# Optimization experiments

Hardware: AMD Instinct MI355X
Metric: run time of the kernel (lower is better)

## Reference

```python
import jax, jax.numpy as jnp
import numpy as np

ROPE_BASE = 10000.0


def _rope(x):
    # Faithful to the torch module: positions indexed by x.shape[2],
    # which after split_heads is the HEADS axis. x: [B, S, H, D]
    B, S, H, D = x.shape
    theta = 1.0 / (ROPE_BASE ** (jnp.arange(0, D, 2, dtype=x.dtype) / D))  # [D/2]
    pos = jnp.arange(H, dtype=x.dtype)[:, None]  # [H, 1]
    ang = pos * theta  # [H, D/2], broadcasts against [B, S, H, D/2]
    sin, cos = jnp.sin(ang), jnp.cos(ang)
    xe, xo = x[..., 0::2], x[..., 1::2]
    re = xe * cos - xo * sin
    ro = xe * sin + xo * cos
    # interleave back: even slots <- re, odd slots <- ro
    return jnp.stack([re, ro], axis=-1).reshape(B, S, H, D)


def setup_inputs() -> dict:
    key = jax.random.key(0)
    k0, k1, k2, k3 = jax.random.split(key, 4)
    B, S, Dm = 8, 2048, 2048
    scale = 1.0 / np.sqrt(Dm)
    return {
        "x": jax.random.normal(k0, (B, S, Dm), dtype=jnp.float32),
        "Wq": jax.random.normal(k1, (Dm, Dm), dtype=jnp.float32) * scale,
        "Wk": jax.random.normal(k2, (Dm, Dm), dtype=jnp.float32) * scale,
        "Wv": jax.random.normal(k3, (Dm, Dm), dtype=jnp.float32) * scale,
        "st_pos": 0,
    }


def reference(x, Wq, Wk, Wv, st_pos):
    B, S, Dm = x.shape
    H = 16
    D = Dm // H  # head_dim = 128
    q = jnp.einsum("bsd,df->bsf", x, Wq).reshape(B, S, H, D)
    k = jnp.einsum("bsd,df->bsf", x, Wk).reshape(B, S, H, D)
    v = jnp.einsum("bsd,df->bsf", x, Wv).reshape(B, S, H, D)
    q = _rope(q)
    k = _rope(k)
    return q, k, v
```

## Files before the change

kernel.cpp:

```cpp
#include <hip/hip_runtime.h>
#include <hip/hip_bf16.h>
#include <stdint.h>


typedef __attribute__((ext_vector_type(8))) short short8;
typedef __attribute__((ext_vector_type(4))) float f32x4;

__device__ __forceinline__ unsigned short f2bf(float f) {
  __bf16 h = (__bf16)f;
  return __builtin_bit_cast(unsigned short, h);
}

__device__ __forceinline__ void gload_lds16(const void* g, void* l) {
  __builtin_amdgcn_global_load_lds((const __attribute__((address_space(1))) void*)g,
                                   (__attribute__((address_space(3))) void*)l,
                                   16, 0, 0);
}


__global__ __launch_bounds__(256) void convert_x(const float* __restrict__ X,
                                                 unsigned short* __restrict__ Xb,
                                                 int n8) {
  const int stride = gridDim.x * blockDim.x;
  for (int i = blockIdx.x * blockDim.x + threadIdx.x; i < n8; i += stride) {
    const float4 v0 = ((const float4*)X)[(size_t)i * 2 + 0];
    const float4 v1 = ((const float4*)X)[(size_t)i * 2 + 1];
    uint4 w;
    w.x = (uint32_t)f2bf(v0.x) | ((uint32_t)f2bf(v0.y) << 16);
    w.y = (uint32_t)f2bf(v0.z) | ((uint32_t)f2bf(v0.w) << 16);
    w.z = (uint32_t)f2bf(v1.x) | ((uint32_t)f2bf(v1.y) << 16);
    w.w = (uint32_t)f2bf(v1.z) | ((uint32_t)f2bf(v1.w) << 16);
    ((uint4*)Xb)[i] = w;
  }
}

__global__ __launch_bounds__(256) void transpose_cvt(const float* __restrict__ W,
                                                     unsigned short* __restrict__ WT) {
  __shared__ unsigned short tile[64][65];
  const int bx = blockIdx.x * 64;
  const int by = blockIdx.y * 64;
  const int t  = threadIdx.x;
  const int tr = t >> 4;
  const int tc = (t & 15) * 4;
#pragma unroll
  for (int i = 0; i < 4; ++i) {
    const int r = tr + i * 16;
    const float4 v = *(const float4*)&W[(size_t)(by + r) * 2048 + bx + tc];
    tile[r][tc + 0] = f2bf(v.x);
    tile[r][tc + 1] = f2bf(v.y);
    tile[r][tc + 2] = f2bf(v.z);
    tile[r][tc + 3] = f2bf(v.w);
  }
  __syncthreads();
#pragma unroll
  for (int i = 0; i < 4; ++i) {
    const int a = tr + i * 16;
    ushort4 o;
    o.x = tile[tc + 0][a];
    o.y = tile[tc + 1][a];
    o.z = tile[tc + 2][a];
    o.w = tile[tc + 3][a];
    *(ushort4*)&WT[(size_t)(bx + a) * 2048 + by + tc] = o;
  }
}


__global__ __launch_bounds__(512, 2) void qkv_fused9(const unsigned short* __restrict__ Xb,
                                                     const unsigned short* __restrict__ WT,
                                                     float* __restrict__ Out) {
  extern __shared__ char smem[];

  const int wg  = blockIdx.x;
  const int swz = (wg & 7) * 192 + (wg >> 3);
  const int mb  = swz / 24, nb = swz % 24;
  const int m0  = mb * 256, n0 = nb * 256;

  const int tid  = threadIdx.x;
  const int wave = tid >> 6, lane = tid & 63;
  const int l15  = lane & 15, lg = lane >> 4;
  const int wm   = (wave >> 2) * 128;
  const int wn   = (wave & 3) * 64;
  const int s0   = ((lg ^ ((l15 >> 1) & 3)) << 4);

  const unsigned short* Xp = Xb + (size_t)m0 * 2048;
  const unsigned short* Wp = WT + (size_t)n0 * 2048;

  const int srow  = tid >> 2;
  const int sswz  = ((tid & 3) ^ ((tid >> 3) & 3)) << 3;

  f32x4 acc[8][4] = {};

#define STAGE(S)                                                              \
  do {                                                                        \
    const int kt_ = (S) * 32;                                                 \
    char* base_ = smem + ((S) & 3) * 32768;                                   \
    _Pragma("unroll") for (int i = 0; i < 2; ++i) {                           \
      const int row = i * 128 + srow;                                         \
      gload_lds16(Xp + (size_t)row * 2048 + kt_ + sswz,                       \
                  base_ + i * 8192 + tid * 16);                               \
    }                                                                         \
    _Pragma("unroll") for (int i = 0; i < 2; ++i) {                           \
      const int row = i * 128 + srow;                                         \
      gload_lds16(Wp + (size_t)row * 2048 + kt_ + sswz,                       \
                  base_ + 16384 + i * 8192 + tid * 16);                       \
    }                                                                         \
  } while (0)

#define BODY(S, VMCNT_ASM, DO_STAGE)                                          \
  do {                                                                        \
    asm volatile(VMCNT_ASM ::: "memory");                                     \
    __builtin_amdgcn_s_barrier();                                             \
    if (DO_STAGE) STAGE((S) + 3);                                             \
    const char* Ab_ = smem + ((S) & 3) * 32768;                               \
    const char* Bb_ = Ab_ + 16384;                                            \
    short8 bf[4], af[8];                                                      \
    _Pragma("unroll") for (int ni = 0; ni < 4; ++ni)                          \
      bf[ni] = *(const short8*)(Bb_ + ((wn + ni * 16 + l15) << 6) + s0);      \
    _Pragma("unroll") for (int mi = 0; mi < 8; ++mi)                          \
      af[mi] = *(const short8*)(Ab_ + ((wm + mi * 16 + l15) << 6) + s0);      \
    __builtin_amdgcn_s_setprio(1);                                            \
    _Pragma("unroll") for (int mi = 0; mi < 8; ++mi)                          \
      _Pragma("unroll") for (int ni = 0; ni < 4; ++ni)                        \
        asm("v_mfma_f32_16x16x32_bf16 %0, %1, %2, %0"                         \
            : "+v"(acc[mi][ni])                                               \
            : "v"(af[mi]), "v"(bf[ni]));                                      \
    __builtin_amdgcn_s_setprio(0);                                            \
  } while (0)

  STAGE(0); STAGE(1); STAGE(2);

  for (int s = 0; s < 61; ++s)
    BODY(s, "s_waitcnt vmcnt(8)", 1);
  BODY(61, "s_waitcnt vmcnt(8)", 0);
  BODY(62, "s_waitcnt vmcnt(4)", 0);
  BODY(63, "s_waitcnt vmcnt(0)", 0);

#undef STAGE
#undef BODY

#pragma unroll
  for (int ni = 0; ni < 4; ++ni) {
    const int col = n0 + wn + ni * 16 + l15;
    const int sec = col >> 11;
    const int lc  = col & 2047;
    float c = 1.0f, ssg = 0.0f;
    if (sec < 2) {
      const int h = lc >> 7;
      const int p = (lc & 127) >> 1;
      const float theta = exp2f(-(float)p * 0.20762050593046014f);
      float s;
      sincosf((float)h * theta, &s, &c);
      ssg = (l15 & 1) ? s : -s;
    }
    float* outp = Out + (size_t)sec * 33554432 + lc;
#pragma unroll
    for (int mi = 0; mi < 8; ++mi) {
      const f32x4 a = acc[mi][ni];
#pragma unroll
      for (int r = 0; r < 4; ++r) {
        const float val = a[r];
        float res = val;
        if (sec < 2) {
          const float other = __shfl_xor(val, 1);
          res = val * c + other * ssg;
        }
        __builtin_nontemporal_store(
            res, outp + (size_t)(m0 + wm + mi * 16 + lg * 4 + r) * 2048);
      }
    }
  }
}

__global__ __launch_bounds__(256) void qkv_gemm_small(const float* __restrict__ X,
                                                      const unsigned short* __restrict__ WTl,
                                                      float* __restrict__ Out,
                                                      const int do_rope) {
  __shared__ unsigned short As[128 * 64];
  __shared__ unsigned short Bs[128 * 64];
  const int t    = threadIdx.x;
  const int wave = t >> 6, lane = t & 63;
  const int l15  = lane & 15, lg = lane >> 4;
  const int wm   = (wave >> 1) * 64;
  const int wn   = (wave & 1) * 64;
  const int m0   = blockIdx.y * 128;
  const int n0   = blockIdx.x * 128;

  f32x4 acc[4][4] = {};

  for (int kt = 0; kt < 2048; kt += 64) {
#pragma unroll
    for (int i = 0; i < 8; ++i) {
      const int f = i * 256 + t;
      const int row = f >> 4, chunk = f & 15;
      const float4 v = *(const float4*)&X[(size_t)(m0 + row) * 2048 + kt + chunk * 4];
      const uint32_t lo = (uint32_t)f2bf(v.x) | ((uint32_t)f2bf(v.y) << 16);
      const uint32_t hi = (uint32_t)f2bf(v.z) | ((uint32_t)f2bf(v.w) << 16);
      const int slot = chunk >> 1;
      const int off  = row * 128 + (((slot ^ (row & 7)) << 4) | ((chunk & 1) << 3));
      uint2* p = (uint2*)((char*)As + off);
      p->x = lo; p->y = hi;
    }
#pragma unroll
    for (int i = 0; i < 4; ++i) {
      const int seg = i * 4 + wave;
      const int row = seg * 8 + (lane >> 3);
      const int ps  = lane & 7;
      const int ss  = ps ^ (row & 7);
      gload_lds16(WTl + (size_t)(n0 + row) * 2048 + kt + ss * 8,
                  (char*)Bs + seg * 1024 + lane * 16);
    }
    __syncthreads();
#pragma unroll
    for (int kk = 0; kk < 2; ++kk) {
      short8 afr[4], bfr[4];
#pragma unroll
      for (int mi = 0; mi < 4; ++mi) {
        const int row  = wm + mi * 16 + l15;
        const int slot = kk * 4 + lg;
        afr[mi] = *(const short8*)((const char*)As + row * 128 + ((slot ^ (row & 7)) << 4));
      }
#pragma unroll
      for (int ni = 0; ni < 4; ++ni) {
        const int row  = wn + ni * 16 + l15;
        const int slot = kk * 4 + lg;
        bfr[ni] = *(const short8*)((const char*)Bs + row * 128 + ((slot ^ (row & 7)) << 4));
      }
#pragma unroll
      for (int mi = 0; mi < 4; ++mi)
#pragma unroll
        for (int ni = 0; ni < 4; ++ni)
          asm("v_mfma_f32_16x16x32_bf16 %0, %1, %2, %0"
              : "+v"(acc[mi][ni])
              : "v"(afr[mi]), "v"(bfr[ni]));
    }
    __syncthreads();
  }

#pragma unroll
  for (int ni = 0; ni < 4; ++ni) {
    const int col = n0 + wn + ni * 16 + l15;
    float c = 1.0f, ssg = 0.0f;
    if (do_rope) {
      const int h = col >> 7;
      const int p = (col & 127) >> 1;
      const float theta = exp2f(-(float)p * 0.20762050593046014f);
      float s;
      sincosf((float)h * theta, &s, &c);
      ssg = (l15 & 1) ? s : -s;
    }
#pragma unroll
    for (int mi = 0; mi < 4; ++mi) {
      const f32x4 a = acc[mi][ni];
#pragma unroll
      for (int r = 0; r < 4; ++r) {
        const float val = a[r];
        float res = val;
        if (do_rope) {
          const float other = __shfl_xor(val, 1);
          res = val * c + other * ssg;
        }
        Out[(size_t)(m0 + wm + mi * 16 + lg * 4 + r) * 2048 + col] = res;
      }
    }
  }
}

extern "C" void kernel_launch(void* const* d_in, const int* in_sizes, int n_in,
                              void* d_out, int out_size, void* d_ws, size_t ws_size,
                              hipStream_t stream) {
  (void)in_sizes; (void)n_in; (void)out_size;
  const float* x  = (const float*)d_in[0];
  const float* Wq = (const float*)d_in[1];
  const float* Wk = (const float*)d_in[2];
  const float* Wv = (const float*)d_in[3];
  float* out = (float*)d_out;

  const size_t XB_ELEMS = 16384ull * 2048;
  const size_t WT_ELEMS = 6144ull * 2048;
  dim3 tb(256), tg(32, 32);

  if (ws_size >= (XB_ELEMS + WT_ELEMS) * sizeof(unsigned short)) {
    unsigned short* Xb  = (unsigned short*)d_ws;
    unsigned short* WTf = Xb + XB_ELEMS;
    convert_x<<<2048, 256, 0, stream>>>(x, Xb, (int)(XB_ELEMS / 8));
    transpose_cvt<<<tg, tb, 0, stream>>>(Wq, WTf);
    transpose_cvt<<<tg, tb, 0, stream>>>(Wk, WTf + 2048ull * 2048);
    transpose_cvt<<<tg, tb, 0, stream>>>(Wv, WTf + 2ull * 2048 * 2048);
    hipFuncSetAttribute((const void*)qkv_fused9,
                        hipFuncAttributeMaxDynamicSharedMemorySize, 131072);
    qkv_fused9<<<1536, 512, 131072, stream>>>(Xb, WTf, out);
  } else {
    unsigned short* WqT = (unsigned short*)d_ws;
    unsigned short* WkT = WqT + 2048ull * 2048;
    unsigned short* WvT = WkT + 2048ull * 2048;
    transpose_cvt<<<tg, tb, 0, stream>>>(Wq, WqT);
    transpose_cvt<<<tg, tb, 0, stream>>>(Wk, WkT);
    transpose_cvt<<<tg, tb, 0, stream>>>(Wv, WvT);
    dim3 gg(16, 128);
    qkv_gemm_small<<<gg, tb, 0, stream>>>(x, WqT, out,            1);
    qkv_gemm_small<<<gg, tb, 0, stream>>>(x, WkT, out + 33554432, 1);
    qkv_gemm_small<<<gg, tb, 0, stream>>>(x, WvT, out + 67108864, 0);
  }
}
```

Measured before the change: 448.2 us.

## Restructure GEMM mainloop into 64-wide K tiles with phased A/B prefetch

```diff
diff --git a/kernel.cpp b/kernel.cpp
--- a/kernel.cpp
+++ b/kernel.cpp
@@ -65,9 +65,9 @@
 }
 
 
-__global__ __launch_bounds__(512, 2) void qkv_fused9(const unsigned short* __restrict__ Xb,
-                                                     const unsigned short* __restrict__ WT,
-                                                     float* __restrict__ Out) {
+__global__ __launch_bounds__(512, 2) void qkv_fused10(const unsigned short* __restrict__ Xb,
+                                                      const unsigned short* __restrict__ WT,
+                                                      float* __restrict__ Out) {
   extern __shared__ char smem[];
 
   const int wg  = blockIdx.x;
@@ -80,63 +80,108 @@
   const int l15  = lane & 15, lg = lane >> 4;
   const int wm   = (wave >> 2) * 128;
   const int wn   = (wave & 3) * 64;
-  const int s0   = ((lg ^ ((l15 >> 1) & 3)) << 4);
+  const int s0   = ((lg ^ (l15 & 7)) << 4);
 
   const unsigned short* Xp = Xb + (size_t)m0 * 2048;
   const unsigned short* Wp = WT + (size_t)n0 * 2048;
 
-  const int srow  = tid >> 2;
-  const int sswz  = ((tid & 3) ^ ((tid >> 3) & 3)) << 3;
+  const int srow  = tid >> 3;
+  const int sslot = tid & 7;
 
   f32x4 acc[8][4] = {};
 
-#define STAGE(S)                                                              \
+#define GLD_A(TP1, H)                                                         \
   do {                                                                        \
-    const int kt_ = (S) * 32;                                                 \
-    char* base_ = smem + ((S) & 3) * 32768;                                   \
-    _Pragma("unroll") for (int i = 0; i < 2; ++i) {                           \
-      const int row = i * 128 + srow;                                         \
-      gload_lds16(Xp + (size_t)row * 2048 + kt_ + sswz,                       \
-                  base_ + i * 8192 + tid * 16);                               \
-    }                                                                         \
-    _Pragma("unroll") for (int i = 0; i < 2; ++i) {                           \
-      const int row = i * 128 + srow;                                         \
-      gload_lds16(Wp + (size_t)row * 2048 + kt_ + sswz,                       \
-                  base_ + 16384 + i * 8192 + tid * 16);                       \
+    char* dst_ = smem + (((TP1) & 1) << 16) + ((H) << 14);                    \
+    _Pragma("unroll") for (int i_ = 0; i_ < 2; ++i_) {                        \
+      const int row_ = (H) * 128 + i_ * 64 + srow;                            \
+      gload_lds16(Xp + (size_t)row_ * 2048 + (TP1) * 64 +                     \
+                      ((sslot ^ (row_ & 7)) << 3),                            \
+                  dst_ + i_ * 8192 + tid * 16);                               \
     }                                                                         \
   } while (0)
 
-#define BODY(S, VMCNT_ASM, DO_STAGE)                                          \
+#define GLD_B(TP2, H)                                                         \
   do {                                                                        \
-    asm volatile(VMCNT_ASM ::: "memory");                                     \
-    __builtin_amdgcn_s_barrier();                                             \
-    if (DO_STAGE) STAGE((S) + 3);                                             \
-    const char* Ab_ = smem + ((S) & 3) * 32768;                               \
-    const char* Bb_ = Ab_ + 16384;                                            \
-    short8 bf[4], af[8];                                                      \
-    _Pragma("unroll") for (int ni = 0; ni < 4; ++ni)                          \
-      bf[ni] = *(const short8*)(Bb_ + ((wn + ni * 16 + l15) << 6) + s0);      \
-    _Pragma("unroll") for (int mi = 0; mi < 8; ++mi)                          \
-      af[mi] = *(const short8*)(Ab_ + ((wm + mi * 16 + l15) << 6) + s0);      \
+    char* dst_ = smem + (((TP2) & 1) << 16) + 32768 + ((H) << 14);            \
+    _Pragma("unroll") for (int i_ = 0; i_ < 2; ++i_) {                        \
+      const int row_ = (H) * 128 + i_ * 64 + srow;                            \
+      gload_lds16(Wp + (size_t)row_ * 2048 + (TP2) * 64 +                     \
+                      ((sslot ^ (row_ & 7)) << 3),                            \
+                  dst_ + i_ * 8192 + tid * 16);                               \
+    }                                                                         \
+  } while (0)
+
+#define LDA4(MH, KS)                                                          \
+  _Pragma("unroll") for (int mi_ = 0; mi_ < 4; ++mi_)                         \
+      af[mi_] = *(const short8*)(Ab + ((wm + (MH) * 64 + mi_ * 16 + l15) << 7)\
+                                  + (s0 ^ ((KS) << 6)));
+
+#define PHASE_SYNC                                                            \
+  __builtin_amdgcn_s_barrier();                                               \
+  asm volatile("s_waitcnt lgkmcnt(0)" ::: "memory");                          \
+  __builtin_amdgcn_sched_barrier(0);
+
+#define MFMA16(MH, KS)                                                        \
+  do {                                                                        \
     __builtin_amdgcn_s_setprio(1);                                            \
-    _Pragma("unroll") for (int mi = 0; mi < 8; ++mi)                          \
-      _Pragma("unroll") for (int ni = 0; ni < 4; ++ni)                        \
+    _Pragma("unroll") for (int mi_ = 0; mi_ < 4; ++mi_)                       \
+      _Pragma("unroll") for (int ni_ = 0; ni_ < 4; ++ni_)                     \
         asm("v_mfma_f32_16x16x32_bf16 %0, %1, %2, %0"                         \
-            : "+v"(acc[mi][ni])                                               \
-            : "v"(af[mi]), "v"(bf[ni]));                                      \
+            : "+v"(acc[(MH) * 4 + mi_][ni_])                                  \
+            : "v"(af[mi_]), "v"(bfr[ni_][KS]));                               \
     __builtin_amdgcn_s_setprio(0);                                            \
   } while (0)
 
-  STAGE(0); STAGE(1); STAGE(2);
-
-  for (int s = 0; s < 61; ++s)
-    BODY(s, "s_waitcnt vmcnt(8)", 1);
-  BODY(61, "s_waitcnt vmcnt(8)", 0);
-  BODY(62, "s_waitcnt vmcnt(4)", 0);
-  BODY(63, "s_waitcnt vmcnt(0)", 0);
-
-#undef STAGE
-#undef BODY
+  GLD_A(0, 0); GLD_A(0, 1);
+  GLD_B(0, 0); GLD_B(0, 1);
+  GLD_B(1, 0); GLD_B(1, 1);
+  asm volatile("s_waitcnt vmcnt(4)" ::: "memory");
+  __builtin_amdgcn_s_barrier();
+
+  for (int t = 0; t < 32; ++t) {
+    const char* Ab = smem + ((t & 1) << 16);
+    const char* Bb = Ab + 32768;
+    short8 bfr[4][2], af[4];
+
+#pragma unroll
+    for (int ni_ = 0; ni_ < 4; ++ni_) {
+      const char* p_ = Bb + ((wn + ni_ * 16 + l15) << 7);
+      bfr[ni_][0] = *(const short8*)(p_ + s0);
+      bfr[ni_][1] = *(const short8*)(p_ + (s0 ^ 64));
+    }
+    LDA4(0, 0);
+    if (t < 31) GLD_A(t + 1, 0);
+    PHASE_SYNC;
+    MFMA16(0, 0);
+    __builtin_amdgcn_s_barrier();
+
+    LDA4(1, 0);
+    if (t < 31) GLD_A(t + 1, 1);
+    PHASE_SYNC;
+    MFMA16(1, 0);
+    __builtin_amdgcn_s_barrier();
+
+    LDA4(0, 1);
+    if (t < 30) GLD_B(t + 2, 0);
+    PHASE_SYNC;
+    MFMA16(0, 1);
+    __builtin_amdgcn_s_barrier();
+
+    LDA4(1, 1);
+    if (t < 30) GLD_B(t + 2, 1);
+    PHASE_SYNC;
+    MFMA16(1, 1);
+    if (t == 30)     asm volatile("s_waitcnt vmcnt(0)" ::: "memory");
+    else if (t < 30) asm volatile("s_waitcnt vmcnt(4)" ::: "memory");
+    __builtin_amdgcn_s_barrier();
+  }
+
+#undef GLD_A
+#undef GLD_B
+#undef LDA4
+#undef PHASE_SYNC
+#undef MFMA16
 
 #pragma unroll
   for (int ni = 0; ni < 4; ++ni) {
@@ -286,9 +331,9 @@
     transpose_cvt<<<tg, tb, 0, stream>>>(Wq, WTf);
     transpose_cvt<<<tg, tb, 0, stream>>>(Wk, WTf + 2048ull * 2048);
     transpose_cvt<<<tg, tb, 0, stream>>>(Wv, WTf + 2ull * 2048 * 2048);
-    hipFuncSetAttribute((const void*)qkv_fused9,
+    hipFuncSetAttribute((const void*)qkv_fused10,
                         hipFuncAttributeMaxDynamicSharedMemorySize, 131072);
-    qkv_fused9<<<1536, 512, 131072, stream>>>(Xb, WTf, out);
+    qkv_fused10<<<1536, 512, 131072, stream>>>(Xb, WTf, out);
   } else {
     unsigned short* WqT = (unsigned short*)d_ws;
     unsigned short* WkT = WqT + 2048ull * 2048;
```

New measurement: 445.0 us. No clear change (-0.7%).
